# Performance work log

Measured on AMD Instinct MI355X. Metric: run time of the kernel, lower is better.

The kernel has to match this reference:

```python
import jax, jax.numpy as jnp
import numpy as np

B, S, D, H = 2, 2048, 512, 8
HID = 512
DH = HID // H  # 64


def setup_inputs() -> dict:
    key = jax.random.key(0)
    ks = jax.random.split(key, 11)
    sc = 0.02
    return {
        "q": jax.random.normal(ks[0], (B, S, D), jnp.float32),
        "k": jax.random.normal(ks[1], (B, S, D), jnp.float32),
        "v": jax.random.normal(ks[2], (B, S, D), jnp.float32),
        "Wq": jax.random.normal(ks[3], (D, HID), jnp.float32) * sc,
        "bq": jnp.zeros((HID,), jnp.float32),
        "Wk": jax.random.normal(ks[4], (D, HID), jnp.float32) * sc,
        "bk": jnp.zeros((HID,), jnp.float32),
        "Wv": jax.random.normal(ks[5], (D, HID), jnp.float32) * sc,
        "bv": jnp.zeros((HID,), jnp.float32),
        "Wo": jax.random.normal(ks[6], (HID, D), jnp.float32) * sc,
        "bo": jnp.zeros((D,), jnp.float32),
    }


def reference(q, k, v, Wq, bq, Wk, bk, Wv, bv, Wo, bo):
    # Linear projections: [B,S,D] -> [B,S,HID]
    qp = q @ Wq + bq
    kp = k @ Wk + bk
    vp = v @ Wv + bv
    # Faithful to torch .view(B, -1, S, head_dim): raw reshape, NOT a
    # [B,S,H,d] transpose. Head i reads a contiguous block of the buffer.
    qh = qp.reshape(B, H, S, DH)
    kh = kp.reshape(B, H, S, DH)
    vh = vp.reshape(B, H, S, DH)
    # scores [B,H,S,S]; NOTE: original divides by sqrt(d) AFTER softmax.
    scores = jnp.einsum("bhsd,bhtd->bhst", qh, kh)
    attn = jax.nn.softmax(scores, axis=-1) / np.sqrt(DH).astype(np.float32)
    ctx = jnp.einsum("bhst,bhtd->bhsd", attn, vh)
    # torch.cat over heads along last dim -> [B,S,H*d] with head blocks
    concat = jnp.transpose(ctx, (0, 2, 1, 3)).reshape(B, S, HID)
    return concat @ Wo + bo
```

## Files before the change

### kernel.cpp

```cpp
#include <hip/hip_runtime.h>
#include <hip/hip_bf16.h>

typedef __bf16 bf16_t;
typedef __bf16 bf16x8 __attribute__((ext_vector_type(8)));
typedef __bf16 bf16x4 __attribute__((ext_vector_type(4)));
typedef short short4v __attribute__((ext_vector_type(4)));
typedef float f32x4 __attribute__((ext_vector_type(4)));

static_assert(sizeof(bf16x8) == 16, "bf16x8 must be 16B");

#define BB 2
#define SS 2048
#define DD 512
#define HH 8
#define DH 64

__global__ void prep(const float* __restrict__ q, const float* __restrict__ k,
                     const float* __restrict__ v, const float* __restrict__ w0,
                     const float* __restrict__ w1, const float* __restrict__ w2,
                     const float* __restrict__ w3, bf16_t* __restrict__ qkvb,
                     bf16_t* __restrict__ wt, int n) {
  const int tid = threadIdx.x;
  if (blockIdx.z < 3) {
    const float* src = (blockIdx.z == 0) ? q : (blockIdx.z == 1) ? k : v;
    bf16_t* out = qkvb + (size_t)blockIdx.z * n;
    int i = (blockIdx.x * 256 + tid) * 8;
    if (i >= n) return;
    const float4* s4 = (const float4*)(src + i);
    float4 a = s4[0], b = s4[1];
    bf16x8 o;
    o[0] = (bf16_t)a.x; o[1] = (bf16_t)a.y; o[2] = (bf16_t)a.z; o[3] = (bf16_t)a.w;
    o[4] = (bf16_t)b.x; o[5] = (bf16_t)b.y; o[6] = (bf16_t)b.z; o[7] = (bf16_t)b.w;
    *(bf16x8*)(out + i) = o;
  } else {
    __shared__ float tile[32][33];
    const int x = blockIdx.x;
    const int wsel = x >> 8;
    const int nb = ((x >> 4) & 15) * 32, kb = (x & 15) * 32;
    const int tx = tid & 31, ty = tid >> 5;
    const float* W = (wsel == 0) ? w0 : (wsel == 1) ? w1 : (wsel == 2) ? w2 : w3;
    bf16_t* out = wt + (size_t)wsel * 512 * 512;
#pragma unroll
    for (int i = 0; i < 4; i++)
      tile[ty + i * 8][tx] = W[(size_t)(kb + ty + i * 8) * 512 + nb + tx];
    __syncthreads();
#pragma unroll
    for (int i = 0; i < 4; i++)
      out[(size_t)(nb + ty + i * 8) * 512 + kb + tx] = (bf16_t)tile[tx][ty + i * 8];
  }
}

template <int BM, int BN, int WM, int WN, typename OutT>
__global__ __launch_bounds__(256) void gemm2(
    const bf16_t* __restrict__ Abase, const bf16_t* __restrict__ Btbase,
    const float* __restrict__ bias0, const float* __restrict__ bias1,
    const float* __restrict__ bias2, OutT* __restrict__ Cbase,
    int M, int N, int K, long Az, long Bz, long Cz) {
  static_assert(BM == 2 * WM && BN == 2 * WN, "2x2 wave grid");
  constexpr int FM = WM / 16, FN = WN / 16;
  constexpr int AJ = BM / 32, BJ = BN / 32;

  const bf16_t* A  = Abase + (size_t)blockIdx.z * Az;
  const bf16_t* Bt = Btbase + (size_t)blockIdx.z * Bz;
  const float* bias = (blockIdx.z == 0) ? bias0 : (blockIdx.z == 1) ? bias1 : bias2;
  OutT* C = Cbase + (size_t)blockIdx.z * Cz;

  __shared__ bf16_t As[2][BM * 64];
  __shared__ bf16_t Bs[2][BN * 64];

  const int tid = threadIdx.x, w = tid >> 6, l = tid & 63;
  const int bm = blockIdx.y, bn = blockIdx.x;
  const int wm0 = (w >> 1) * WM, wn0 = (w & 1) * WN;
  const int lr = l & 15, lg = l >> 4;

  f32x4 acc[FM][FN] = {};

  auto stage = [&](int buf, int kt) {
#pragma unroll
    for (int j = 0; j < AJ; j++) {
      int lin = j * 256 + tid;
      int row = lin >> 3, cc = lin & 7;
      const bf16_t* g = A + (size_t)(bm * BM + row) * K + kt * 64 + cc * 8;
      __builtin_amdgcn_global_load_lds(
          (const __attribute__((address_space(1))) void*)g,
          (__attribute__((address_space(3))) void*)(&As[buf][(j * 256 + w * 64) * 8]), 16, 0, 0);
    }
#pragma unroll
    for (int j = 0; j < BJ; j++) {
      int lin = j * 256 + tid;
      int row = lin >> 3, cc = lin & 7;
      const bf16_t* g = Bt + (size_t)(bn * BN + row) * K + kt * 64 + cc * 8;
      __builtin_amdgcn_global_load_lds(
          (const __attribute__((address_space(1))) void*)g,
          (__attribute__((address_space(3))) void*)(&Bs[buf][(j * 256 + w * 64) * 8]), 16, 0, 0);
    }
  };

  stage(0, 0);
  const int KT = K >> 6;
  for (int kt = 0; kt < KT; kt++) {
    __syncthreads();
    if (kt + 1 < KT) stage((kt + 1) & 1, kt + 1);
    const bf16_t* as = As[kt & 1];
    const bf16_t* bs = Bs[kt & 1];
#pragma unroll
    for (int kc = 0; kc < 2; kc++) {
      bf16x8 a[FM], b[FN];
#pragma unroll
      for (int i = 0; i < FM; i++)
        a[i] = *(const bf16x8*)(as + (wm0 + i * 16 + lr) * 64 + kc * 32 + lg * 8);
#pragma unroll
      for (int j = 0; j < FN; j++)
        b[j] = *(const bf16x8*)(bs + (wn0 + j * 16 + lr) * 64 + kc * 32 + lg * 8);
#pragma unroll
      for (int i = 0; i < FM; i++)
#pragma unroll
        for (int j = 0; j < FN; j++)
          acc[i][j] = __builtin_amdgcn_mfma_f32_16x16x32_bf16(a[i], b[j], acc[i][j], 0, 0, 0);
    }
  }

  const int row0 = bm * BM + wm0, col0 = bn * BN + wn0;
#pragma unroll
  for (int j = 0; j < FN; j++) {
    int col = col0 + j * 16 + lr;
    float bv = bias[col];
#pragma unroll
    for (int i = 0; i < FM; i++) {
      int row = row0 + i * 16 + lg * 4;
#pragma unroll
      for (int r = 0; r < 4; r++) {
        float vv = acc[i][j][r] + bv;
        C[(size_t)(row + r) * N + col] = (OutT)vv;
      }
    }
  }
}

__global__ __launch_bounds__(256) void attn_flash(const bf16_t* __restrict__ qp,
                                                  const bf16_t* __restrict__ kp,
                                                  const bf16_t* __restrict__ vp,
                                                  float* __restrict__ Opart,
                                                  float* __restrict__ mlpart) {
  const int id = blockIdx.x;
  const int bh = (id & 7) | (((id >> 3) & 1) << 3);
  const int qt = (id >> 4) & 31;
  const int half = id >> 9;
  const int pidx = (((qt << 4) | bh) << 1) + half;

  const int tid = threadIdx.x, w = tid >> 6, l = tid & 63;
  const int lr = l & 15, lg = l >> 4;
  const size_t hb = (size_t)bh * (SS * DH);
  const bf16_t* Q = qp + hb;
  const bf16_t* Kh = kp + hb;
  const bf16_t* Vh = vp + hb;

  __shared__ __align__(16) bf16_t KsL[2][4096];
  __shared__ __align__(16) bf16_t VtL[2][4096];

  const int qr0 = qt * 64 + w * 16;

  bf16x8 aq[2];
#pragma unroll
  for (int kc = 0; kc < 2; kc++)
    aq[kc] = *(const bf16x8*)(Q + (size_t)(qr0 + lr) * DH + kc * 32 + lg * 8);

  f32x4 o[4] = {};
  float m_run = -1e30f, l_run = 0.f;

  const int krow = (w << 3) + (l >> 3);
  const int kcol = ((l & 7) ^ (l >> 3)) << 3;
  const bf16_t* ks_it = Kh + (size_t)(half * 16) * 4096 + krow * 64 + kcol;

  auto stage_k = [&](int buf, const bf16_t* ks) {
    char* kb = (char*)&KsL[buf][0];
    __builtin_amdgcn_global_load_lds((const __attribute__((address_space(1))) void*)ks,
        (__attribute__((address_space(3))) void*)(kb + (w << 10)), 16, 0, 0);
    __builtin_amdgcn_global_load_lds((const __attribute__((address_space(1))) void*)(ks + 2048),
        (__attribute__((address_space(3))) void*)(kb + 4096 + (w << 10)), 16, 0, 0);
  };

  const int vk0 = l, vd0 = w;
  const int vd1 = 4 + w;
  bf16x8 vreg0, vreg1;
  auto load_v = [&](int it) {
    const size_t kv0 = (size_t)it * 64;
    vreg0 = *(const bf16x8*)(Vh + (kv0 + vk0) * DH + vd0 * 8);
    vreg1 = *(const bf16x8*)(Vh + (kv0 + vk0) * DH + vd1 * 8);
  };
  auto write_v = [&](int buf) {
    char* vt = (char*)&VtL[buf][0];
#pragma unroll
    for (int j = 0; j < 8; j++) {
      int d0 = vd0 * 8 + j;
      *(bf16_t*)(vt + d0 * 128 + ((vk0 * 2) ^ (j << 4))) = vreg0[j];
    }
#pragma unroll
    for (int j = 0; j < 8; j++) {
      int d1 = vd1 * 8 + j;
      *(bf16_t*)(vt + d1 * 128 + ((vk0 * 2) ^ (j << 4))) = vreg1[j];
    }
  };

  stage_k(0, ks_it);
  load_v(half * 16);
  write_v(0);

  for (int i = 0; i < 16; i++) {
    const int buf = i & 1;
    __syncthreads();
    if (i + 1 < 16) {
      ks_it += 4096;
      stage_k(buf ^ 1, ks_it);
      load_v(half * 16 + i + 1);
    }

    const char* ksb = (const char*)&KsL[buf][0];
    f32x4 s[4] = {};
    __builtin_amdgcn_s_setprio(1);
#pragma unroll
    for (int kc = 0; kc < 2; kc++) {
#pragma unroll
      for (int n = 0; n < 4; n++) {
        bf16x8 bk = *(const bf16x8*)(ksb + (n * 16 + lr) * 128 +
                                     ((kc * 64 + lg * 16) ^ ((lr & 7) << 4)));
        s[n] = __builtin_amdgcn_mfma_f32_16x16x32_bf16(bk, aq[kc], s[n], 0, 0, 0);
      }
    }
    __builtin_amdgcn_s_setprio(0);

    float pmax = -1e30f;
#pragma unroll
    for (int n = 0; n < 4; n++)
#pragma unroll
      for (int r = 0; r < 4; r++) pmax = fmaxf(pmax, s[n][r]);
    pmax = fmaxf(pmax, __shfl_xor(pmax, 16));
    pmax = fmaxf(pmax, __shfl_xor(pmax, 32));
    if (!__all(pmax <= m_run + 8.0f)) {
      float mnew = fmaxf(m_run, pmax);
      float scale = __expf(m_run - mnew);
      l_run *= scale;
#pragma unroll
      for (int n = 0; n < 4; n++)
#pragma unroll
        for (int r = 0; r < 4; r++) o[n][r] *= scale;
      m_run = mnew;
    }
    float rs = 0.f;
#pragma unroll
    for (int n = 0; n < 4; n++)
#pragma unroll
      for (int r = 0; r < 4; r++) {
        float e = __expf(s[n][r] - m_run);
        s[n][r] = e;
        rs += e;
      }
    rs += __shfl_xor(rs, 16);
    rs += __shfl_xor(rs, 32);
    l_run += rs;

    short4v pb[4];
#pragma unroll
    for (int c2 = 0; c2 < 4; c2++) {
      bf16x4 t;
#pragma unroll
      for (int r = 0; r < 4; r++) t[r] = (bf16_t)s[c2][r];
      pb[c2] = __builtin_bit_cast(short4v, t);
    }
    const char* vtb = (const char*)&VtL[buf][0];
    __builtin_amdgcn_s_setprio(1);
#pragma unroll
    for (int n = 0; n < 4; n++) {
#pragma unroll
      for (int c2 = 0; c2 < 4; c2++) {
        bf16x4 bvh = *(const bf16x4*)(vtb + (n * 16 + lr) * 128 +
                                      ((c2 * 32 + lg * 8) ^ ((lr & 7) << 4)));
        o[n] = __builtin_amdgcn_mfma_f32_16x16x16bf16_1k(
            __builtin_bit_cast(short4v, bvh), pb[c2], o[n], 0, 0, 0);
      }
    }
    __builtin_amdgcn_s_setprio(0);

    if (i + 1 < 16) write_v(buf ^ 1);
  }

  float* ob = Opart + (size_t)pidx * 4096;
#pragma unroll
  for (int n = 0; n < 4; n++)
    *(f32x4*)(ob + ((w * 4 + n) * 64 + l) * 4) = o[n];
  if (lg == 0) {
    mlpart[(size_t)pidx * 128 + (w * 16 + lr) * 2 + 0] = m_run;
    mlpart[(size_t)pidx * 128 + (w * 16 + lr) * 2 + 1] = l_run;
  }
}

__global__ __launch_bounds__(256) void attn_combine(const float* __restrict__ Opart,
                                                    const float* __restrict__ mlpart,
                                                    bf16_t* __restrict__ ctx) {
  const int id = blockIdx.x;
  const int qt = id >> 4, bh = id & 15;
  const int t = threadIdx.x, w = t >> 6, l = t & 63;
  const int lr = l & 15, lg = l >> 4;
  const int p0 = id * 2, p1 = id * 2 + 1;
  const int q = w * 16 + lr;

  float m1 = mlpart[(size_t)p0 * 128 + q * 2 + 0];
  float l1 = mlpart[(size_t)p0 * 128 + q * 2 + 1];
  float m2 = mlpart[(size_t)p1 * 128 + q * 2 + 0];
  float l2 = mlpart[(size_t)p1 * 128 + q * 2 + 1];
  float m = fmaxf(m1, m2);
  float e1 = __expf(m1 - m), e2 = __expf(m2 - m);
  float denom = (l1 * e1 + l2 * e2) * 8.0f;
  float f1 = e1 / denom, f2 = e2 / denom;

  const int b = bh >> 3, h = bh & 7;
  const int trow = qt * 64 + q;
  size_t rowbase = ((size_t)b * SS + trow) * 512 + h * 64;

  const float* oa = Opart + (size_t)p0 * 4096;
  const float* obp = Opart + (size_t)p1 * 4096;
#pragma unroll
  for (int n = 0; n < 4; n++) {
    f32x4 a = *(const f32x4*)(oa + ((w * 4 + n) * 64 + l) * 4);
    f32x4 b2 = *(const f32x4*)(obp + ((w * 4 + n) * 64 + l) * 4);
    bf16x4 ov;
#pragma unroll
    for (int r = 0; r < 4; r++) ov[r] = (bf16_t)(a[r] * f1 + b2[r] * f2);
    *(bf16x4*)(&ctx[rowbase + n * 16 + lg * 4]) = ov;
  }
}

extern "C" void kernel_launch(void* const* d_in, const int* in_sizes, int n_in,
                              void* d_out, int out_size, void* d_ws, size_t ws_size,
                              hipStream_t stream) {
  const float* q  = (const float*)d_in[0];
  const float* k  = (const float*)d_in[1];
  const float* v  = (const float*)d_in[2];
  const float* Wq = (const float*)d_in[3];
  const float* bq = (const float*)d_in[4];
  const float* Wk = (const float*)d_in[5];
  const float* bk = (const float*)d_in[6];
  const float* Wv = (const float*)d_in[7];
  const float* bv = (const float*)d_in[8];
  const float* Wo = (const float*)d_in[9];
  const float* bo = (const float*)d_in[10];

  const size_t NQKV = (size_t)4096 * 512;
  const size_t NW = (size_t)512 * 512;

  bf16_t* ws   = (bf16_t*)d_ws;
  bf16_t* wt   = ws;
  bf16_t* proj = wt + 4 * NW;
  bf16_t* ctx  = proj + 3 * NQKV;
  bf16_t* qkvb = ctx + NQKV;
  float* Opart  = (float*)qkvb;
  float* mlpart = Opart + (size_t)1024 * 4096;

  prep<<<dim3(1024, 1, 4), 256, 0, stream>>>(q, k, v, Wq, Wk, Wv, Wo, qkvb, wt, (int)NQKV);
  gemm2<128, 64, 64, 32, bf16_t><<<dim3(8, 32, 3), 256, 0, stream>>>(
      qkvb, wt, bq, bk, bv, proj, 4096, 512, 512, (long)NQKV, (long)NW, (long)NQKV);
  attn_flash<<<1024, 256, 0, stream>>>(proj, proj + NQKV, proj + 2 * NQKV, Opart, mlpart);
  attn_combine<<<512, 256, 0, stream>>>(Opart, mlpart, ctx);
  gemm2<64, 64, 32, 32, float><<<dim3(8, 64, 1), 256, 0, stream>>>(
      ctx, wt + 3 * NW, bo, bo, bo, (float*)d_out, 4096, 512, 512, 0, 0, 0);
}
```

Baseline: 90.41 us.

## Software-pipeline QK^T and PV in flash attention, fold log2e into Q projection

Restructures the attention main loop so that the QK^T MFMAs for tile T are issued alongside the softmax and PV work of tile T-1, using two score register sets and a triple-buffered V^T shared-memory tile. This lets matrix work overlap the exp/max vector work. Log2(e) is folded into the Q projection epilogue so softmax can use exp2f instead of __expf. The per-iteration row-sum shuffles are deferred to a single reduction after the loop. The cost is more registers and more LDS, which may lower occupancy.

New measurement: 95.47 us. 5.6% more time.

```diff
diff --git a/kernel.cpp b/kernel.cpp
--- a/kernel.cpp
+++ b/kernel.cpp
@@ -14,6 +14,7 @@
 #define DD 512
 #define HH 8
 #define DH 64
+#define LOG2E 1.44269504088896f
 
 __global__ void prep(const float* __restrict__ q, const float* __restrict__ k,
                      const float* __restrict__ v, const float* __restrict__ w0,
@@ -55,7 +56,7 @@
     const bf16_t* __restrict__ Abase, const bf16_t* __restrict__ Btbase,
     const float* __restrict__ bias0, const float* __restrict__ bias1,
     const float* __restrict__ bias2, OutT* __restrict__ Cbase,
-    int M, int N, int K, long Az, long Bz, long Cz) {
+    int M, int N, int K, long Az, long Bz, long Cz, float scale0) {
   static_assert(BM == 2 * WM && BN == 2 * WN, "2x2 wave grid");
   constexpr int FM = WM / 16, FN = WN / 16;
   constexpr int AJ = BM / 32, BJ = BN / 32;
@@ -64,6 +65,7 @@
   const bf16_t* Bt = Btbase + (size_t)blockIdx.z * Bz;
   const float* bias = (blockIdx.z == 0) ? bias0 : (blockIdx.z == 1) ? bias1 : bias2;
   OutT* C = Cbase + (size_t)blockIdx.z * Cz;
+  const float osc = (blockIdx.z == 0) ? scale0 : 1.0f;
 
   __shared__ bf16_t As[2][BM * 64];
   __shared__ bf16_t Bs[2][BN * 64];
@@ -130,7 +132,7 @@
       int row = row0 + i * 16 + lg * 4;
 #pragma unroll
       for (int r = 0; r < 4; r++) {
-        float vv = acc[i][j][r] + bv;
+        float vv = (acc[i][j][r] + bv) * osc;
         C[(size_t)(row + r) * N + col] = (OutT)vv;
       }
     }
@@ -156,7 +158,7 @@
   const bf16_t* Vh = vp + hb;
 
   __shared__ __align__(16) bf16_t KsL[2][4096];
-  __shared__ __align__(16) bf16_t VtL[2][4096];
+  __shared__ __align__(16) bf16_t VtL[3][4096];
 
   const int qr0 = qt * 64 + w * 16;
 
@@ -202,87 +204,100 @@
     }
   };
 
+  const int it0 = half * 16;
   stage_k(0, ks_it);
-  load_v(half * 16);
+  load_v(it0);
   write_v(0);
 
-  for (int i = 0; i < 16; i++) {
-    const int buf = i & 1;
+  f32x4 sA[4], sB[4];
+
+#pragma unroll
+  for (int T = 0; T <= 16; T++) {
     __syncthreads();
-    if (i + 1 < 16) {
+
+    if (T < 16) {
+      f32x4* sc = (T & 1) ? sB : sA;
+      const char* ksb = (const char*)&KsL[T & 1][0];
+#pragma unroll
+      for (int n = 0; n < 4; n++) sc[n] = f32x4{0.f, 0.f, 0.f, 0.f};
+      __builtin_amdgcn_s_setprio(1);
+#pragma unroll
+      for (int kc = 0; kc < 2; kc++) {
+#pragma unroll
+        for (int n = 0; n < 4; n++) {
+          bf16x8 bk = *(const bf16x8*)(ksb + (n * 16 + lr) * 128 +
+                                       ((kc * 64 + lg * 16) ^ ((lr & 7) << 4)));
+          sc[n] = __builtin_amdgcn_mfma_f32_16x16x32_bf16(bk, aq[kc], sc[n], 0, 0, 0);
+        }
+      }
+      __builtin_amdgcn_s_setprio(0);
+    }
+
+    if (T + 1 < 16) {
       ks_it += 4096;
-      stage_k(buf ^ 1, ks_it);
-      load_v(half * 16 + i + 1);
-    }
-
-    const char* ksb = (const char*)&KsL[buf][0];
-    f32x4 s[4] = {};
-    __builtin_amdgcn_s_setprio(1);
-#pragma unroll
-    for (int kc = 0; kc < 2; kc++) {
+      stage_k((T + 1) & 1, ks_it);
+      load_v(it0 + T + 1);
+    }
+
+    if (T >= 1) {
+      f32x4* sp = (T & 1) ? sA : sB;
+
+      float pmax = -1e30f;
+#pragma unroll
+      for (int n = 0; n < 4; n++)
+#pragma unroll
+        for (int r = 0; r < 4; r++) pmax = fmaxf(pmax, sp[n][r]);
+      pmax = fmaxf(pmax, __shfl_xor(pmax, 16));
+      pmax = fmaxf(pmax, __shfl_xor(pmax, 32));
+      if (!__all(pmax <= m_run + 8.0f)) {
+        float mnew = fmaxf(m_run, pmax);
+        float scale = exp2f(m_run - mnew);
+        l_run *= scale;
+#pragma unroll
+        for (int n = 0; n < 4; n++)
+#pragma unroll
+          for (int r = 0; r < 4; r++) o[n][r] *= scale;
+        m_run = mnew;
+      }
+      float rs = 0.f;
+#pragma unroll
+      for (int n = 0; n < 4; n++)
+#pragma unroll
+        for (int r = 0; r < 4; r++) {
+          float e = exp2f(sp[n][r] - m_run);
+          sp[n][r] = e;
+          rs += e;
+        }
+      l_run += rs;
+
+      short4v pb[4];
+#pragma unroll
+      for (int c2 = 0; c2 < 4; c2++) {
+        bf16x4 t;
+#pragma unroll
+        for (int r = 0; r < 4; r++) t[r] = (bf16_t)sp[c2][r];
+        pb[c2] = __builtin_bit_cast(short4v, t);
+      }
+      const char* vtb = (const char*)&VtL[(T - 1) % 3][0];
+      __builtin_amdgcn_s_setprio(1);
 #pragma unroll
       for (int n = 0; n < 4; n++) {
-        bf16x8 bk = *(const bf16x8*)(ksb + (n * 16 + lr) * 128 +
-                                     ((kc * 64 + lg * 16) ^ ((lr & 7) << 4)));
-        s[n] = __builtin_amdgcn_mfma_f32_16x16x32_bf16(bk, aq[kc], s[n], 0, 0, 0);
-      }
-    }
-    __builtin_amdgcn_s_setprio(0);
-
-    float pmax = -1e30f;
-#pragma unroll
-    for (int n = 0; n < 4; n++)
-#pragma unroll
-      for (int r = 0; r < 4; r++) pmax = fmaxf(pmax, s[n][r]);
-    pmax = fmaxf(pmax, __shfl_xor(pmax, 16));
-    pmax = fmaxf(pmax, __shfl_xor(pmax, 32));
-    if (!__all(pmax <= m_run + 8.0f)) {
-      float mnew = fmaxf(m_run, pmax);
-      float scale = __expf(m_run - mnew);
-      l_run *= scale;
-#pragma unroll
-      for (int n = 0; n < 4; n++)
-#pragma unroll
-        for (int r = 0; r < 4; r++) o[n][r] *= scale;
-      m_run = mnew;
-    }
-    float rs = 0.f;
-#pragma unroll
-    for (int n = 0; n < 4; n++)
-#pragma unroll
-      for (int r = 0; r < 4; r++) {
-        float e = __expf(s[n][r] - m_run);
-        s[n][r] = e;
-        rs += e;
-      }
-    rs += __shfl_xor(rs, 16);
-    rs += __shfl_xor(rs, 32);
-    l_run += rs;
-
-    short4v pb[4];
-#pragma unroll
-    for (int c2 = 0; c2 < 4; c2++) {
-      bf16x4 t;
-#pragma unroll
-      for (int r = 0; r < 4; r++) t[r] = (bf16_t)s[c2][r];
-      pb[c2] = __builtin_bit_cast(short4v, t);
-    }
-    const char* vtb = (const char*)&VtL[buf][0];
-    __builtin_amdgcn_s_setprio(1);
-#pragma unroll
-    for (int n = 0; n < 4; n++) {
-#pragma unroll
-      for (int c2 = 0; c2 < 4; c2++) {
-        bf16x4 bvh = *(const bf16x4*)(vtb + (n * 16 + lr) * 128 +
-                                      ((c2 * 32 + lg * 8) ^ ((lr & 7) << 4)));
-        o[n] = __builtin_amdgcn_mfma_f32_16x16x16bf16_1k(
-            __builtin_bit_cast(short4v, bvh), pb[c2], o[n], 0, 0, 0);
-      }
-    }
-    __builtin_amdgcn_s_setprio(0);
-
-    if (i + 1 < 16) write_v(buf ^ 1);
-  }
+#pragma unroll
+        for (int c2 = 0; c2 < 4; c2++) {
+          bf16x4 bvh = *(const bf16x4*)(vtb + (n * 16 + lr) * 128 +
+                                        ((c2 * 32 + lg * 8) ^ ((lr & 7) << 4)));
+          o[n] = __builtin_amdgcn_mfma_f32_16x16x16bf16_1k(
+              __builtin_bit_cast(short4v, bvh), pb[c2], o[n], 0, 0, 0);
+        }
+      }
+      __builtin_amdgcn_s_setprio(0);
+    }
+
+    if (T + 1 < 16) write_v((T + 1) % 3);
+  }
+
+  l_run += __shfl_xor(l_run, 16);
+  l_run += __shfl_xor(l_run, 32);
 
   float* ob = Opart + (size_t)pidx * 4096;
 #pragma unroll
@@ -309,7 +324,7 @@
   float m2 = mlpart[(size_t)p1 * 128 + q * 2 + 0];
   float l2 = mlpart[(size_t)p1 * 128 + q * 2 + 1];
   float m = fmaxf(m1, m2);
-  float e1 = __expf(m1 - m), e2 = __expf(m2 - m);
+  float e1 = exp2f(m1 - m), e2 = exp2f(m2 - m);
   float denom = (l1 * e1 + l2 * e2) * 8.0f;
   float f1 = e1 / denom, f2 = e2 / denom;
 
@@ -358,9 +373,9 @@
 
   prep<<<dim3(1024, 1, 4), 256, 0, stream>>>(q, k, v, Wq, Wk, Wv, Wo, qkvb, wt, (int)NQKV);
   gemm2<128, 64, 64, 32, bf16_t><<<dim3(8, 32, 3), 256, 0, stream>>>(
-      qkvb, wt, bq, bk, bv, proj, 4096, 512, 512, (long)NQKV, (long)NW, (long)NQKV);
+      qkvb, wt, bq, bk, bv, proj, 4096, 512, 512, (long)NQKV, (long)NW, (long)NQKV, LOG2E);
   attn_flash<<<1024, 256, 0, stream>>>(proj, proj + NQKV, proj + 2 * NQKV, Opart, mlpart);
   attn_combine<<<512, 256, 0, stream>>>(Opart, mlpart, ctx);
   gemm2<64, 64, 32, 32, float><<<dim3(8, 64, 1), 256, 0, stream>>>(
-      ctx, wt + 3 * NW, bo, bo, bo, (float*)d_out, 4096, 512, 512, 0, 0, 0);
-}
+      ctx, wt + 3 * NW, bo, bo, bo, (float*)d_out, 4096, 512, 512, 0, 0, 0, 1.0f);
+}
```

## Emit V pre-transposed and swizzled from projection GEMM; fold log2e into Q

Applied to the files above, without the earlier changes.

The QKV projection GEMM now writes V directly in a transposed, XOR-swizzled per-tile layout, so the attention kernel can stage V with asynchronous global-to-LDS loads like K. This removes the per-iteration register load and scalar LDS transpose writes of V. Q is prescaled by log2(e) so the softmax can use exp2f, and the row-sum shuffles move out of the loop to run once at the end. The GEMM epilogue for V becomes scattered 2-byte global stores, and Q rounding to bf16 now happens after the scaling.

Result: slower. 100.2 us (+10.8%).

```diff
diff --git a/kernel.cpp b/kernel.cpp
--- a/kernel.cpp
+++ b/kernel.cpp
@@ -14,6 +14,7 @@
 #define DD 512
 #define HH 8
 #define DH 64
+#define LOG2E 1.44269504088896f
 
 __global__ void prep(const float* __restrict__ q, const float* __restrict__ k,
                      const float* __restrict__ v, const float* __restrict__ w0,
@@ -50,12 +51,13 @@
   }
 }
 
-template <int BM, int BN, int WM, int WN, typename OutT>
+template <int BM, int BN, int WM, int WN, int TMODE, typename OutT>
 __global__ __launch_bounds__(256) void gemm2(
     const bf16_t* __restrict__ Abase, const bf16_t* __restrict__ Btbase,
     const float* __restrict__ bias0, const float* __restrict__ bias1,
     const float* __restrict__ bias2, OutT* __restrict__ Cbase,
-    int M, int N, int K, long Az, long Bz, long Cz) {
+    bf16_t* __restrict__ Tbase,
+    int M, int N, int K, long Az, long Bz, long Cz, float scale0) {
   static_assert(BM == 2 * WM && BN == 2 * WN, "2x2 wave grid");
   constexpr int FM = WM / 16, FN = WN / 16;
   constexpr int AJ = BM / 32, BJ = BN / 32;
@@ -64,6 +66,7 @@
   const bf16_t* Bt = Btbase + (size_t)blockIdx.z * Bz;
   const float* bias = (blockIdx.z == 0) ? bias0 : (blockIdx.z == 1) ? bias1 : bias2;
   OutT* C = Cbase + (size_t)blockIdx.z * Cz;
+  const float osc = (blockIdx.z == 0) ? scale0 : 1.0f;
 
   __shared__ bf16_t As[2][BM * 64];
   __shared__ bf16_t Bs[2][BN * 64];
@@ -121,6 +124,31 @@
   }
 
   const int row0 = bm * BM + wm0, col0 = bn * BN + wn0;
+  if (TMODE && blockIdx.z == 2) {
+    const int brow = bm * BM;
+    char* vbase = (char*)(Tbase +
+        (size_t)((brow >> 11) * 8 + ((brow & 2047) >> 8)) * (SS * DH));
+    const int sbase = (brow & 255) + wm0 + lg * 4;
+#pragma unroll
+    for (int j = 0; j < FN; j++) {
+      int d = wn0 + j * 16 + lr;
+      float bv = bias[bn * 64 + d];
+      const int dsw = (d & 7) << 4;
+      char* drow = vbase + d * 128;
+#pragma unroll
+      for (int i = 0; i < FM; i++) {
+#pragma unroll
+        for (int r = 0; r < 4; r++) {
+          int s = sbase + i * 16 + r;
+          int tile = s >> 3;
+          int kv = ((s & 7) << 3) | bn;
+          *(bf16_t*)(drow + tile * 8192 + ((kv << 1) ^ dsw)) =
+              (bf16_t)(acc[i][j][r] + bv);
+        }
+      }
+    }
+    return;
+  }
 #pragma unroll
   for (int j = 0; j < FN; j++) {
     int col = col0 + j * 16 + lr;
@@ -130,7 +158,7 @@
       int row = row0 + i * 16 + lg * 4;
 #pragma unroll
       for (int r = 0; r < 4; r++) {
-        float vv = acc[i][j][r] + bv;
+        float vv = (acc[i][j][r] + bv) * osc;
         C[(size_t)(row + r) * N + col] = (OutT)vv;
       }
     }
@@ -139,7 +167,7 @@
 
 __global__ __launch_bounds__(256) void attn_flash(const bf16_t* __restrict__ qp,
                                                   const bf16_t* __restrict__ kp,
-                                                  const bf16_t* __restrict__ vp,
+                                                  const bf16_t* __restrict__ vtp,
                                                   float* __restrict__ Opart,
                                                   float* __restrict__ mlpart) {
   const int id = blockIdx.x;
@@ -153,7 +181,7 @@
   const size_t hb = (size_t)bh * (SS * DH);
   const bf16_t* Q = qp + hb;
   const bf16_t* Kh = kp + hb;
-  const bf16_t* Vh = vp + hb;
+  const bf16_t* Vth = vtp + hb;
 
   __shared__ __align__(16) bf16_t KsL[2][4096];
   __shared__ __align__(16) bf16_t VtL[2][4096];
@@ -168,52 +196,30 @@
   f32x4 o[4] = {};
   float m_run = -1e30f, l_run = 0.f;
 
-  const int krow = (w << 3) + (l >> 3);
-  const int kcol = ((l & 7) ^ (l >> 3)) << 3;
-  const bf16_t* ks_it = Kh + (size_t)(half * 16) * 4096 + krow * 64 + kcol;
-
-  auto stage_k = [&](int buf, const bf16_t* ks) {
+  const int srow = (w << 3) + (l >> 3);
+  const int scol = ((l & 7) ^ (l >> 3)) << 3;
+  const bf16_t* ks_it = Kh + (size_t)(half * 16) * 4096 + srow * 64 + scol;
+  const bf16_t* vs_it = Vth + (size_t)(half * 16) * 4096 + (w * 64 + l) * 8;
+
+  auto stage = [&](int buf) {
     char* kb = (char*)&KsL[buf][0];
-    __builtin_amdgcn_global_load_lds((const __attribute__((address_space(1))) void*)ks,
+    char* vb = (char*)&VtL[buf][0];
+    __builtin_amdgcn_global_load_lds((const __attribute__((address_space(1))) void*)ks_it,
         (__attribute__((address_space(3))) void*)(kb + (w << 10)), 16, 0, 0);
-    __builtin_amdgcn_global_load_lds((const __attribute__((address_space(1))) void*)(ks + 2048),
+    __builtin_amdgcn_global_load_lds((const __attribute__((address_space(1))) void*)(ks_it + 2048),
         (__attribute__((address_space(3))) void*)(kb + 4096 + (w << 10)), 16, 0, 0);
+    __builtin_amdgcn_global_load_lds((const __attribute__((address_space(1))) void*)vs_it,
+        (__attribute__((address_space(3))) void*)(vb + (w << 10)), 16, 0, 0);
+    __builtin_amdgcn_global_load_lds((const __attribute__((address_space(1))) void*)(vs_it + 2048),
+        (__attribute__((address_space(3))) void*)(vb + 4096 + (w << 10)), 16, 0, 0);
   };
 
-  const int vk0 = l, vd0 = w;
-  const int vd1 = 4 + w;
-  bf16x8 vreg0, vreg1;
-  auto load_v = [&](int it) {
-    const size_t kv0 = (size_t)it * 64;
-    vreg0 = *(const bf16x8*)(Vh + (kv0 + vk0) * DH + vd0 * 8);
-    vreg1 = *(const bf16x8*)(Vh + (kv0 + vk0) * DH + vd1 * 8);
-  };
-  auto write_v = [&](int buf) {
-    char* vt = (char*)&VtL[buf][0];
-#pragma unroll
-    for (int j = 0; j < 8; j++) {
-      int d0 = vd0 * 8 + j;
-      *(bf16_t*)(vt + d0 * 128 + ((vk0 * 2) ^ (j << 4))) = vreg0[j];
-    }
-#pragma unroll
-    for (int j = 0; j < 8; j++) {
-      int d1 = vd1 * 8 + j;
-      *(bf16_t*)(vt + d1 * 128 + ((vk0 * 2) ^ (j << 4))) = vreg1[j];
-    }
-  };
-
-  stage_k(0, ks_it);
-  load_v(half * 16);
-  write_v(0);
+  stage(0);
 
   for (int i = 0; i < 16; i++) {
     const int buf = i & 1;
     __syncthreads();
-    if (i + 1 < 16) {
-      ks_it += 4096;
-      stage_k(buf ^ 1, ks_it);
-      load_v(half * 16 + i + 1);
-    }
+    if (i + 1 < 16) { ks_it += 4096; vs_it += 4096; stage(buf ^ 1); }
 
     const char* ksb = (const char*)&KsL[buf][0];
     f32x4 s[4] = {};
@@ -238,7 +244,7 @@
     pmax = fmaxf(pmax, __shfl_xor(pmax, 32));
     if (!__all(pmax <= m_run + 8.0f)) {
       float mnew = fmaxf(m_run, pmax);
-      float scale = __expf(m_run - mnew);
+      float scale = exp2f(m_run - mnew);
       l_run *= scale;
 #pragma unroll
       for (int n = 0; n < 4; n++)
@@ -251,12 +257,10 @@
     for (int n = 0; n < 4; n++)
 #pragma unroll
       for (int r = 0; r < 4; r++) {
-        float e = __expf(s[n][r] - m_run);
+        float e = exp2f(s[n][r] - m_run);
         s[n][r] = e;
         rs += e;
       }
-    rs += __shfl_xor(rs, 16);
-    rs += __shfl_xor(rs, 32);
     l_run += rs;
 
     short4v pb[4];
@@ -280,9 +284,10 @@
       }
     }
     __builtin_amdgcn_s_setprio(0);
-
-    if (i + 1 < 16) write_v(buf ^ 1);
-  }
+  }
+
+  l_run += __shfl_xor(l_run, 16);
+  l_run += __shfl_xor(l_run, 32);
 
   float* ob = Opart + (size_t)pidx * 4096;
 #pragma unroll
@@ -309,7 +314,7 @@
   float m2 = mlpart[(size_t)p1 * 128 + q * 2 + 0];
   float l2 = mlpart[(size_t)p1 * 128 + q * 2 + 1];
   float m = fmaxf(m1, m2);
-  float e1 = __expf(m1 - m), e2 = __expf(m2 - m);
+  float e1 = exp2f(m1 - m), e2 = exp2f(m2 - m);
   float denom = (l1 * e1 + l2 * e2) * 8.0f;
   float f1 = e1 / denom, f2 = e2 / denom;
 
@@ -351,16 +356,17 @@
   bf16_t* ws   = (bf16_t*)d_ws;
   bf16_t* wt   = ws;
   bf16_t* proj = wt + 4 * NW;
-  bf16_t* ctx  = proj + 3 * NQKV;
+  bf16_t* vtp  = proj + 2 * NQKV;
+  bf16_t* ctx  = vtp + NQKV;
   bf16_t* qkvb = ctx + NQKV;
   float* Opart  = (float*)qkvb;
   float* mlpart = Opart + (size_t)1024 * 4096;
 
   prep<<<dim3(1024, 1, 4), 256, 0, stream>>>(q, k, v, Wq, Wk, Wv, Wo, qkvb, wt, (int)NQKV);
-  gemm2<128, 64, 64, 32, bf16_t><<<dim3(8, 32, 3), 256, 0, stream>>>(
-      qkvb, wt, bq, bk, bv, proj, 4096, 512, 512, (long)NQKV, (long)NW, (long)NQKV);
-  attn_flash<<<1024, 256, 0, stream>>>(proj, proj + NQKV, proj + 2 * NQKV, Opart, mlpart);
+  gemm2<128, 64, 64, 32, 1, bf16_t><<<dim3(8, 32, 3), 256, 0, stream>>>(
+      qkvb, wt, bq, bk, bv, proj, vtp, 4096, 512, 512, (long)NQKV, (long)NW, (long)NQKV, LOG2E);
+  attn_flash<<<1024, 256, 0, stream>>>(proj, proj + NQKV, vtp, Opart, mlpart);
   attn_combine<<<512, 256, 0, stream>>>(Opart, mlpart, ctx);
-  gemm2<64, 64, 32, 32, float><<<dim3(8, 64, 1), 256, 0, stream>>>(
-      ctx, wt + 3 * NW, bo, bo, bo, (float*)d_out, 4096, 512, 512, 0, 0, 0);
-}
+  gemm2<64, 64, 32, 32, 0, float><<<dim3(8, 64, 1), 256, 0, stream>>>(
+      ctx, wt + 3 * NW, bo, bo, bo, (float*)d_out, nullptr, 4096, 512, 512, 0, 0, 0, 1.0f);
+}
```

## Split attention KV into quarters with bf16 partials and exp2 softmax

Applied to the files above, without the earlier changes.

Flash attention now splits the key range into four parts instead of two and processes 32-key tiles. This doubles the block count, halves the LDS footprint, and adds an occupancy hint of 8 blocks per CU. Partial outputs are stored as bf16 to cut combine traffic, and the combine kernel merges four partials. Q is prescaled by log2(e) in the projection epilogue so exp2f replaces __expf, and the row-sum shuffle reduction moves out of the loop to the end. The trade-offs are more partial-output writes, extra combine work and bf16 rounding of the partials.

New measurement: 91.14 us. About the same (+0.8%).

```diff
diff --git a/kernel.cpp b/kernel.cpp
--- a/kernel.cpp
+++ b/kernel.cpp
@@ -14,6 +14,7 @@
 #define DD 512
 #define HH 8
 #define DH 64
+#define LOG2E 1.44269504088896f
 
 __global__ void prep(const float* __restrict__ q, const float* __restrict__ k,
                      const float* __restrict__ v, const float* __restrict__ w0,
@@ -55,7 +56,7 @@
     const bf16_t* __restrict__ Abase, const bf16_t* __restrict__ Btbase,
     const float* __restrict__ bias0, const float* __restrict__ bias1,
     const float* __restrict__ bias2, OutT* __restrict__ Cbase,
-    int M, int N, int K, long Az, long Bz, long Cz) {
+    int M, int N, int K, long Az, long Bz, long Cz, float scale0) {
   static_assert(BM == 2 * WM && BN == 2 * WN, "2x2 wave grid");
   constexpr int FM = WM / 16, FN = WN / 16;
   constexpr int AJ = BM / 32, BJ = BN / 32;
@@ -64,6 +65,7 @@
   const bf16_t* Bt = Btbase + (size_t)blockIdx.z * Bz;
   const float* bias = (blockIdx.z == 0) ? bias0 : (blockIdx.z == 1) ? bias1 : bias2;
   OutT* C = Cbase + (size_t)blockIdx.z * Cz;
+  const float osc = (blockIdx.z == 0) ? scale0 : 1.0f;
 
   __shared__ bf16_t As[2][BM * 64];
   __shared__ bf16_t Bs[2][BN * 64];
@@ -130,23 +132,23 @@
       int row = row0 + i * 16 + lg * 4;
 #pragma unroll
       for (int r = 0; r < 4; r++) {
-        float vv = acc[i][j][r] + bv;
+        float vv = (acc[i][j][r] + bv) * osc;
         C[(size_t)(row + r) * N + col] = (OutT)vv;
       }
     }
   }
 }
 
-__global__ __launch_bounds__(256) void attn_flash(const bf16_t* __restrict__ qp,
-                                                  const bf16_t* __restrict__ kp,
-                                                  const bf16_t* __restrict__ vp,
-                                                  float* __restrict__ Opart,
-                                                  float* __restrict__ mlpart) {
+__global__ __launch_bounds__(256, 8) void attn_flash(const bf16_t* __restrict__ qp,
+                                                     const bf16_t* __restrict__ kp,
+                                                     const bf16_t* __restrict__ vp,
+                                                     bf16_t* __restrict__ Opart,
+                                                     float* __restrict__ mlpart) {
   const int id = blockIdx.x;
   const int bh = (id & 7) | (((id >> 3) & 1) << 3);
   const int qt = (id >> 4) & 31;
-  const int half = id >> 9;
-  const int pidx = (((qt << 4) | bh) << 1) + half;
+  const int quarter = id >> 9;
+  const int pidx = (((qt << 4) | bh) << 2) + quarter;
 
   const int tid = threadIdx.x, w = tid >> 6, l = tid & 63;
   const int lr = l & 15, lg = l >> 4;
@@ -155,8 +157,8 @@
   const bf16_t* Kh = kp + hb;
   const bf16_t* Vh = vp + hb;
 
-  __shared__ __align__(16) bf16_t KsL[2][4096];
-  __shared__ __align__(16) bf16_t VtL[2][4096];
+  __shared__ __align__(16) bf16_t KsL[2][2048];
+  __shared__ __align__(16) bf16_t VtL[2][2048];
 
   const int qr0 = qt * 64 + w * 16;
 
@@ -170,58 +172,50 @@
 
   const int krow = (w << 3) + (l >> 3);
   const int kcol = ((l & 7) ^ (l >> 3)) << 3;
-  const bf16_t* ks_it = Kh + (size_t)(half * 16) * 4096 + krow * 64 + kcol;
+  const bf16_t* ks_it = Kh + (size_t)(quarter * 16) * 2048 + krow * 64 + kcol;
 
   auto stage_k = [&](int buf, const bf16_t* ks) {
     char* kb = (char*)&KsL[buf][0];
     __builtin_amdgcn_global_load_lds((const __attribute__((address_space(1))) void*)ks,
         (__attribute__((address_space(3))) void*)(kb + (w << 10)), 16, 0, 0);
-    __builtin_amdgcn_global_load_lds((const __attribute__((address_space(1))) void*)(ks + 2048),
-        (__attribute__((address_space(3))) void*)(kb + 4096 + (w << 10)), 16, 0, 0);
   };
 
-  const int vk0 = l, vd0 = w;
-  const int vd1 = 4 + w;
-  bf16x8 vreg0, vreg1;
+  const int vkv = l & 31;
+  const int vdv = (w << 1) | (l >> 5);
+  bf16x8 vreg;
   auto load_v = [&](int it) {
-    const size_t kv0 = (size_t)it * 64;
-    vreg0 = *(const bf16x8*)(Vh + (kv0 + vk0) * DH + vd0 * 8);
-    vreg1 = *(const bf16x8*)(Vh + (kv0 + vk0) * DH + vd1 * 8);
+    vreg = *(const bf16x8*)(Vh + ((size_t)it * 32 + vkv) * DH + vdv * 8);
   };
   auto write_v = [&](int buf) {
     char* vt = (char*)&VtL[buf][0];
 #pragma unroll
     for (int j = 0; j < 8; j++) {
-      int d0 = vd0 * 8 + j;
-      *(bf16_t*)(vt + d0 * 128 + ((vk0 * 2) ^ (j << 4))) = vreg0[j];
-    }
-#pragma unroll
-    for (int j = 0; j < 8; j++) {
-      int d1 = vd1 * 8 + j;
-      *(bf16_t*)(vt + d1 * 128 + ((vk0 * 2) ^ (j << 4))) = vreg1[j];
+      int d = vdv * 8 + j;
+      *(bf16_t*)(vt + d * 64 + ((vkv << 1) ^ (j << 3))) = vreg[j];
     }
   };
 
+  const int it0 = quarter * 16;
   stage_k(0, ks_it);
-  load_v(half * 16);
+  load_v(it0);
   write_v(0);
 
   for (int i = 0; i < 16; i++) {
     const int buf = i & 1;
     __syncthreads();
     if (i + 1 < 16) {
-      ks_it += 4096;
+      ks_it += 2048;
       stage_k(buf ^ 1, ks_it);
-      load_v(half * 16 + i + 1);
+      load_v(it0 + i + 1);
     }
 
     const char* ksb = (const char*)&KsL[buf][0];
-    f32x4 s[4] = {};
+    f32x4 s[2] = {};
     __builtin_amdgcn_s_setprio(1);
 #pragma unroll
     for (int kc = 0; kc < 2; kc++) {
 #pragma unroll
-      for (int n = 0; n < 4; n++) {
+      for (int n = 0; n < 2; n++) {
         bf16x8 bk = *(const bf16x8*)(ksb + (n * 16 + lr) * 128 +
                                      ((kc * 64 + lg * 16) ^ ((lr & 7) << 4)));
         s[n] = __builtin_amdgcn_mfma_f32_16x16x32_bf16(bk, aq[kc], s[n], 0, 0, 0);
@@ -231,14 +225,14 @@
 
     float pmax = -1e30f;
 #pragma unroll
-    for (int n = 0; n < 4; n++)
+    for (int n = 0; n < 2; n++)
 #pragma unroll
       for (int r = 0; r < 4; r++) pmax = fmaxf(pmax, s[n][r]);
     pmax = fmaxf(pmax, __shfl_xor(pmax, 16));
     pmax = fmaxf(pmax, __shfl_xor(pmax, 32));
     if (!__all(pmax <= m_run + 8.0f)) {
       float mnew = fmaxf(m_run, pmax);
-      float scale = __expf(m_run - mnew);
+      float scale = exp2f(m_run - mnew);
       l_run *= scale;
 #pragma unroll
       for (int n = 0; n < 4; n++)
@@ -248,20 +242,18 @@
     }
     float rs = 0.f;
 #pragma unroll
-    for (int n = 0; n < 4; n++)
+    for (int n = 0; n < 2; n++)
 #pragma unroll
       for (int r = 0; r < 4; r++) {
-        float e = __expf(s[n][r] - m_run);
+        float e = exp2f(s[n][r] - m_run);
         s[n][r] = e;
         rs += e;
       }
-    rs += __shfl_xor(rs, 16);
-    rs += __shfl_xor(rs, 32);
     l_run += rs;
 
-    short4v pb[4];
-#pragma unroll
-    for (int c2 = 0; c2 < 4; c2++) {
+    short4v pb[2];
+#pragma unroll
+    for (int c2 = 0; c2 < 2; c2++) {
       bf16x4 t;
 #pragma unroll
       for (int r = 0; r < 4; r++) t[r] = (bf16_t)s[c2][r];
@@ -270,13 +262,13 @@
     const char* vtb = (const char*)&VtL[buf][0];
     __builtin_amdgcn_s_setprio(1);
 #pragma unroll
-    for (int n = 0; n < 4; n++) {
-#pragma unroll
-      for (int c2 = 0; c2 < 4; c2++) {
-        bf16x4 bvh = *(const bf16x4*)(vtb + (n * 16 + lr) * 128 +
-                                      ((c2 * 32 + lg * 8) ^ ((lr & 7) << 4)));
-        o[n] = __builtin_amdgcn_mfma_f32_16x16x16bf16_1k(
-            __builtin_bit_cast(short4v, bvh), pb[c2], o[n], 0, 0, 0);
+    for (int nd = 0; nd < 4; nd++) {
+#pragma unroll
+      for (int c2 = 0; c2 < 2; c2++) {
+        bf16x4 bvh = *(const bf16x4*)(vtb + (nd * 16 + lr) * 64 +
+                                      ((c2 * 32 + lg * 8) ^ ((lr & 7) << 3)));
+        o[nd] = __builtin_amdgcn_mfma_f32_16x16x16bf16_1k(
+            __builtin_bit_cast(short4v, bvh), pb[c2], o[nd], 0, 0, 0);
       }
     }
     __builtin_amdgcn_s_setprio(0);
@@ -284,48 +276,65 @@
     if (i + 1 < 16) write_v(buf ^ 1);
   }
 
-  float* ob = Opart + (size_t)pidx * 4096;
-#pragma unroll
-  for (int n = 0; n < 4; n++)
-    *(f32x4*)(ob + ((w * 4 + n) * 64 + l) * 4) = o[n];
+  l_run += __shfl_xor(l_run, 16);
+  l_run += __shfl_xor(l_run, 32);
+
+  bf16_t* ob = Opart + (size_t)pidx * 4096;
+#pragma unroll
+  for (int n = 0; n < 4; n++) {
+    bf16x4 t;
+#pragma unroll
+    for (int r = 0; r < 4; r++) t[r] = (bf16_t)o[n][r];
+    *(bf16x4*)(ob + ((w * 4 + n) * 64 + l) * 4) = t;
+  }
   if (lg == 0) {
     mlpart[(size_t)pidx * 128 + (w * 16 + lr) * 2 + 0] = m_run;
     mlpart[(size_t)pidx * 128 + (w * 16 + lr) * 2 + 1] = l_run;
   }
 }
 
-__global__ __launch_bounds__(256) void attn_combine(const float* __restrict__ Opart,
+__global__ __launch_bounds__(256) void attn_combine(const bf16_t* __restrict__ Opart,
                                                     const float* __restrict__ mlpart,
                                                     bf16_t* __restrict__ ctx) {
-  const int id = blockIdx.x;
-  const int qt = id >> 4, bh = id & 15;
+  const int gid = blockIdx.x;
+  const int qt = gid >> 4, bh = gid & 15;
   const int t = threadIdx.x, w = t >> 6, l = t & 63;
   const int lr = l & 15, lg = l >> 4;
-  const int p0 = id * 2, p1 = id * 2 + 1;
   const int q = w * 16 + lr;
 
-  float m1 = mlpart[(size_t)p0 * 128 + q * 2 + 0];
-  float l1 = mlpart[(size_t)p0 * 128 + q * 2 + 1];
-  float m2 = mlpart[(size_t)p1 * 128 + q * 2 + 0];
-  float l2 = mlpart[(size_t)p1 * 128 + q * 2 + 1];
-  float m = fmaxf(m1, m2);
-  float e1 = __expf(m1 - m), e2 = __expf(m2 - m);
-  float denom = (l1 * e1 + l2 * e2) * 8.0f;
-  float f1 = e1 / denom, f2 = e2 / denom;
+  float mv[4], lv[4];
+#pragma unroll
+  for (int s = 0; s < 4; s++) {
+    const float* ml = mlpart + (size_t)(gid * 4 + s) * 128 + q * 2;
+    mv[s] = ml[0];
+    lv[s] = ml[1];
+  }
+  float m = fmaxf(fmaxf(mv[0], mv[1]), fmaxf(mv[2], mv[3]));
+  float e[4], denom = 0.f;
+#pragma unroll
+  for (int s = 0; s < 4; s++) { e[s] = exp2f(mv[s] - m); denom += lv[s] * e[s]; }
+  denom *= 8.0f;
+  float f[4];
+#pragma unroll
+  for (int s = 0; s < 4; s++) f[s] = e[s] / denom;
 
   const int b = bh >> 3, h = bh & 7;
   const int trow = qt * 64 + q;
   size_t rowbase = ((size_t)b * SS + trow) * 512 + h * 64;
 
-  const float* oa = Opart + (size_t)p0 * 4096;
-  const float* obp = Opart + (size_t)p1 * 4096;
 #pragma unroll
   for (int n = 0; n < 4; n++) {
-    f32x4 a = *(const f32x4*)(oa + ((w * 4 + n) * 64 + l) * 4);
-    f32x4 b2 = *(const f32x4*)(obp + ((w * 4 + n) * 64 + l) * 4);
+    float acc[4] = {0.f, 0.f, 0.f, 0.f};
+#pragma unroll
+    for (int s = 0; s < 4; s++) {
+      bf16x4 v = *(const bf16x4*)(Opart + (size_t)(gid * 4 + s) * 4096 +
+                                  ((w * 4 + n) * 64 + l) * 4);
+#pragma unroll
+      for (int r = 0; r < 4; r++) acc[r] += (float)v[r] * f[s];
+    }
     bf16x4 ov;
 #pragma unroll
-    for (int r = 0; r < 4; r++) ov[r] = (bf16_t)(a[r] * f1 + b2[r] * f2);
+    for (int r = 0; r < 4; r++) ov[r] = (bf16_t)acc[r];
     *(bf16x4*)(&ctx[rowbase + n * 16 + lg * 4]) = ov;
   }
 }
@@ -353,14 +362,14 @@
   bf16_t* proj = wt + 4 * NW;
   bf16_t* ctx  = proj + 3 * NQKV;
   bf16_t* qkvb = ctx + NQKV;
-  float* Opart  = (float*)qkvb;
-  float* mlpart = Opart + (size_t)1024 * 4096;
+  bf16_t* Opart = qkvb;
+  float* mlpart = (float*)(Opart + (size_t)2048 * 4096);
 
   prep<<<dim3(1024, 1, 4), 256, 0, stream>>>(q, k, v, Wq, Wk, Wv, Wo, qkvb, wt, (int)NQKV);
   gemm2<128, 64, 64, 32, bf16_t><<<dim3(8, 32, 3), 256, 0, stream>>>(
-      qkvb, wt, bq, bk, bv, proj, 4096, 512, 512, (long)NQKV, (long)NW, (long)NQKV);
-  attn_flash<<<1024, 256, 0, stream>>>(proj, proj + NQKV, proj + 2 * NQKV, Opart, mlpart);
+      qkvb, wt, bq, bk, bv, proj, 4096, 512, 512, (long)NQKV, (long)NW, (long)NQKV, LOG2E);
+  attn_flash<<<2048, 256, 0, stream>>>(proj, proj + NQKV, proj + 2 * NQKV, Opart, mlpart);
   attn_combine<<<512, 256, 0, stream>>>(Opart, mlpart, ctx);
   gemm2<64, 64, 32, 32, float><<<dim3(8, 64, 1), 256, 0, stream>>>(
-      ctx, wt + 3 * NW, bo, bo, bo, (float*)d_out, 4096, 512, 512, 0, 0, 0);
-}
+      ctx, wt + 3 * NW, bo, bo, bo, (float*)d_out, 4096, 512, 512, 0, 0, 0, 1.0f);
+}
```
